# Performance work log

Measured on AMD Instinct MI355X. Metric: run time of the kernel, lower is better.

The kernel has to match this reference:

```python
import jax, jax.numpy as jnp
import numpy as np

EPS = 1e-12
TEMPERATURE = 0.1
QUEUE_SIZE = 1024
CUTOFF_KM = 25.0
EARTH_R_KM = 6371.0088


def _normalize(x, axis=-1):
    n = jnp.linalg.norm(x, axis=axis, keepdims=True)
    return x / jnp.maximum(n, EPS)


def _haversine_km(a, b):
    # a: (B,1,2), b: (1,S,2) in degrees (lat, lon) -> (B,S) km
    ra, rb = jnp.deg2rad(a), jnp.deg2rad(b)
    dlat = rb[..., 0] - ra[..., 0]
    dlon = rb[..., 1] - ra[..., 1]
    h = jnp.sin(dlat / 2) ** 2 + jnp.cos(ra[..., 0]) * jnp.cos(rb[..., 0]) * jnp.sin(dlon / 2) ** 2
    return 2.0 * EARTH_R_KM * jnp.arcsin(jnp.sqrt(jnp.clip(h, 0.0, 1.0)))


def setup_inputs() -> dict:
    key = jax.random.key(0)
    k1, k2, k3, k4, k5 = jax.random.split(key, 5)
    A, B, F, S = 3, 256, 512, 100000
    V = jax.random.normal(k1, (A, B, F), dtype=jnp.float32)
    L = jax.random.normal(k2, (B, F), dtype=jnp.float32)
    # gps as (lat, lon) degrees
    gps = jax.random.uniform(k3, (B, 2), dtype=jnp.float32) * jnp.array([120.0, 360.0]) - jnp.array([60.0, 180.0])
    support_feats = jax.random.normal(k4, (S, F), dtype=jnp.float32)
    support_gps = jax.random.uniform(k5, (S, 2), dtype=jnp.float32) * jnp.array([120.0, 360.0]) - jnp.array([60.0, 180.0])
    return {"V": V, "L": L, "gps": gps, "support_feats": support_feats, "support_gps": support_gps}


def reference(V, L, gps, support_feats, support_gps):
    T, Q = TEMPERATURE, QUEUE_SIZE
    L_norm = _normalize(L, axis=1)                      # (B,F)
    org = _normalize(V[0] * L_norm, axis=1)             # (B,F)
    aug = _normalize(V[1:] * L_norm, axis=2)            # (A-1,B,F)

    # nearest_neighbours (no_grad): per-batch NN in support set by dot-product sim
    sims = jnp.einsum('sf,bf->sb', support_feats, org)  # (S,B)
    nn_idx = jnp.argmax(sims, axis=0)                   # (B,)
    nn = _normalize(support_feats[nn_idx], axis=1)      # (B,F)
    nn = jax.lax.stop_gradient(nn)

    pos = jnp.exp(jnp.einsum('abf,bf->ab', aug, nn) / T)  # (A-1,B)
    batch_den = jnp.sum(pos, axis=0)                       # (B,)

    # nn_negative_queue (no_grad): first Q support rows farther than 25 km, zeros if fewer
    dist = _haversine_km(gps[:, None, :], support_gps[None, :, :])  # (B,S)
    far = dist > CUTOFF_KM                                          # (B,S)
    order = jnp.argsort(jnp.logical_not(far), axis=1)[:, :Q]        # stable: far rows first, in order
    valid = jnp.take_along_axis(far, order, axis=1)                 # (B,Q)
    negq = jnp.where(valid[..., None], support_feats[order], 0.0)   # (B,Q,F)
    negq = jax.lax.stop_gradient(_normalize(negq, axis=2))          # zero rows stay zero

    queue_den = jnp.sum(jnp.exp(jnp.einsum('bqf,bf->bq', negq, nn) / T), axis=1)  # (B,)

    loss = jnp.mean(-batch_den / (batch_den + queue_den))
    return loss
```

## Files before the change

kernel.cpp:

```cpp
#include <hip/hip_runtime.h>
#include <hip/hip_bf16.h>
#include <math.h>

#define B_N 256
#define F_N 512
#define S_N 100000
#define Q_N 1024
#define EPSF 1e-12f
#define BM 128
#define NBLK ((S_N + BM - 1) / BM)

typedef __attribute__((ext_vector_type(8))) short short8v;
typedef __attribute__((ext_vector_type(4))) float f32x4;

__device__ __forceinline__ unsigned short f2bf(float x) {
  unsigned u = __float_as_uint(x);
  u = u + 0x7FFFu + ((u >> 16) & 1u);
  return (unsigned short)(u >> 16);
}
__device__ __forceinline__ float bf2f(unsigned short h) {
  return __uint_as_float(((unsigned)h) << 16);
}

__device__ __forceinline__ float warpReduceSum(float v) {
  #pragma unroll
  for (int o = 32; o > 0; o >>= 1) v += __shfl_down(v, o);
  return v;
}

__device__ __forceinline__ float blockReduceSum256(float v, float* buf) {
  v = warpReduceSum(v);
  int lane = threadIdx.x & 63, w = threadIdx.x >> 6;
  __syncthreads();
  if (lane == 0) buf[w] = v;
  __syncthreads();
  return buf[0] + buf[1] + buf[2] + buf[3];
}

__device__ __forceinline__ void async_copy16(void* lds, const void* g) {
  __builtin_amdgcn_global_load_lds(
      (const __attribute__((address_space(1))) unsigned int*)g,
      (__attribute__((address_space(3))) unsigned int*)lds, 16, 0, 0);
}

__device__ __forceinline__ void cvt8(const float4 a, const float4 b,
                                     short8v& hi, short8v& lo) {
  union { unsigned u[4]; short8v v; } H, L;
  float xs[8] = {a.x, a.y, a.z, a.w, b.x, b.y, b.z, b.w};
  #pragma unroll
  for (int i = 0; i < 4; ++i) {
    float p = xs[2 * i], q = xs[2 * i + 1];
    union { __hip_bfloat162 b2; unsigned u; } c;
    c.b2 = __float22bfloat162_rn(make_float2(p, q));
    H.u[i] = c.u;
    float rp = p - __uint_as_float(c.u << 16);
    float rq = q - __uint_as_float(c.u & 0xFFFF0000u);
    union { __hip_bfloat162 b2; unsigned u; } d;
    d.b2 = __float22bfloat162_rn(make_float2(rp, rq));
    L.u[i] = d.u;
  }
  hi = H.v; lo = L.v;
}

__global__ __launch_bounds__(256) void k_prep(const float* __restrict__ V,
    const float* __restrict__ L, unsigned short* __restrict__ orgst,
    float* __restrict__ aug) {
  __shared__ float buf[4];
  int b = blockIdx.x, t = threadIdx.x;
  const float2 lv = *(const float2*)&L[b * F_N + t * 2];
  float ss = blockReduceSum256(lv.x * lv.x + lv.y * lv.y, buf);
  float invL = 1.0f / fmaxf(sqrtf(ss), EPSF);
  float lnx = lv.x * invL, lny = lv.y * invL;
  #pragma unroll
  for (int a = 0; a < 3; ++a) {
    const float2 vv = *(const float2*)&V[(a * B_N + b) * F_N + t * 2];
    float yx = vv.x * lnx, yy = vv.y * lny;
    float s2 = blockReduceSum256(yx * yx + yy * yy, buf);
    float inv = 1.0f / fmaxf(sqrtf(s2), EPSF);
    if (a == 0) {
      float ox = yx * inv, oy = yy * inv;
      int f = t * 2;
      int kt = f >> 5, kk = f & 31, sub = kk >> 3, pos = kk & 7;
      unsigned short hx = f2bf(ox), hy = f2bf(oy);
      unsigned short lx = f2bf(ox - bf2f(hx)), ly = f2bf(oy - bf2f(hy));
      int base = kt * 16384 + b * 64;
      ushort2 hv; hv.x = hx; hv.y = hy;
      ushort2 lw; lw.x = lx; lw.y = ly;
      *(ushort2*)&orgst[base + ((sub ^ (b & 7)) << 3) + pos] = hv;
      *(ushort2*)&orgst[base + (((sub | 4) ^ (b & 7)) << 3) + pos] = lw;
    } else {
      float* dst = &aug[((a - 1) * B_N + b) * F_N + t * 2];
      dst[0] = yx * inv;
      dst[1] = yy * inv;
    }
  }
}

__global__ __launch_bounds__(256, 2) void k_sims(const float* __restrict__ support,
    const unsigned short* __restrict__ orgst, unsigned long long* __restrict__ keys) {
  __shared__ __align__(16) unsigned char smem[65536];

  int t = threadIdx.x;
  int lane = t & 63, w = t >> 6;
  int r15 = lane & 15, ks = lane >> 4;
  int s0 = blockIdx.x * BM;

  f32x4 acc0[16], acc1[16];
  #pragma unroll
  for (int n = 0; n < 16; ++n) {
    acc0[n] = (f32x4){0.f, 0.f, 0.f, 0.f};
    acc1[n] = (f32x4){0.f, 0.f, 0.f, 0.f};
  }

  int row0 = s0 + w * 32 + r15;
  int row1 = row0 + 16;
  if (row0 > S_N - 1) row0 = S_N - 1;
  if (row1 > S_N - 1) row1 = S_N - 1;
  const float* ap0 = support + (size_t)row0 * F_N + ks * 8;
  const float* ap1 = support + (size_t)row1 * F_N + ks * 8;

  {
    const unsigned char* src = (const unsigned char*)orgst + t * 16;
    unsigned char* dst = smem + t * 16;
    #pragma unroll
    for (int p = 0; p < 8; ++p) async_copy16(dst + p * 4096, src + p * 4096);
  }
  float4 a0a = *(const float4*)(ap0);
  float4 a0b = *(const float4*)(ap0 + 4);
  float4 a1a = *(const float4*)(ap1);
  float4 a1b = *(const float4*)(ap1 + 4);
  __syncthreads();

  const int hioff = (ks ^ (r15 & 7)) << 4;
  const int looff = ((ks | 4) ^ (r15 & 7)) << 4;

  #pragma unroll 1
  for (int kt = 0; kt < 16; ++kt) {
    const int cur = kt & 1;
    unsigned char* bbuf = smem + cur * 32768;
    if (kt < 15) {
      const unsigned char* src =
          (const unsigned char*)orgst + (kt + 1) * 32768 + t * 16;
      unsigned char* dst = smem + (cur ^ 1) * 32768 + t * 16;
      #pragma unroll
      for (int p = 0; p < 8; ++p) async_copy16(dst + p * 4096, src + p * 4096);
    }
    short8v ah0, al0, ah1, al1;
    cvt8(a0a, a0b, ah0, al0);
    cvt8(a1a, a1b, ah1, al1);
    if (kt < 15) {
      a0a = *(const float4*)(ap0 + (kt + 1) * 32);
      a0b = *(const float4*)(ap0 + (kt + 1) * 32 + 4);
      a1a = *(const float4*)(ap1 + (kt + 1) * 32);
      a1b = *(const float4*)(ap1 + (kt + 1) * 32 + 4);
    }
    const unsigned char* bp = bbuf + r15 * 128 + hioff;
    const unsigned char* bq = bbuf + r15 * 128 + looff;
    #pragma unroll
    for (int n = 0; n < 16; ++n) {
      short8v bh = *(const short8v*)(bp + n * 2048);
      short8v bl = *(const short8v*)(bq + n * 2048);
      acc0[n] = __builtin_amdgcn_mfma_f32_16x16x32_bf16(ah0, bh, acc0[n], 0, 0, 0);
      acc1[n] = __builtin_amdgcn_mfma_f32_16x16x32_bf16(ah1, bh, acc1[n], 0, 0, 0);
      acc0[n] = __builtin_amdgcn_mfma_f32_16x16x32_bf16(al0, bh, acc0[n], 0, 0, 0);
      acc1[n] = __builtin_amdgcn_mfma_f32_16x16x32_bf16(al1, bh, acc1[n], 0, 0, 0);
      acc0[n] = __builtin_amdgcn_mfma_f32_16x16x32_bf16(ah0, bl, acc0[n], 0, 0, 0);
      acc1[n] = __builtin_amdgcn_mfma_f32_16x16x32_bf16(ah1, bl, acc1[n], 0, 0, 0);
    }
    __syncthreads();
  }

  unsigned long long* wk = (unsigned long long*)smem;
  #pragma unroll
  for (int n = 0; n < 16; ++n) {
    float bv = -INFINITY;
    int bi = 0x7FFFFFFF;
    #pragma unroll
    for (int r = 0; r < 4; ++r) {
      int sA = s0 + w * 32 + ks * 4 + r;
      float vA = acc0[n][r];
      if (sA < S_N && (vA > bv || (vA == bv && sA < bi))) { bv = vA; bi = sA; }
      int sB = sA + 16;
      float vB = acc1[n][r];
      if (sB < S_N && (vB > bv || (vB == bv && sB < bi))) { bv = vB; bi = sB; }
    }
    #pragma unroll
    for (int mask = 16; mask <= 32; mask <<= 1) {
      float ov = __shfl_xor(bv, mask);
      int oi = __shfl_xor(bi, mask);
      if (ov > bv || (ov == bv && oi < bi)) { bv = ov; bi = oi; }
    }
    if (lane < 16) {
      unsigned u = __float_as_uint(bv);
      u = (u & 0x80000000u) ? ~u : (u | 0x80000000u);
      wk[w * 256 + n * 16 + lane] =
          ((unsigned long long)u << 32) |
          (unsigned long long)(0xFFFFFFFFu - (unsigned)bi);
    }
  }
  __syncthreads();
  {
    unsigned long long k0 = wk[t], k1 = wk[256 + t];
    unsigned long long k2 = wk[512 + t], k3 = wk[768 + t];
    unsigned long long m01 = k0 > k1 ? k0 : k1;
    unsigned long long m23 = k2 > k3 ? k2 : k3;
    atomicMax(&keys[t], m01 > m23 ? m01 : m23);
  }
}

__global__ __launch_bounds__(256) void k_nn(const float* __restrict__ support,
    const unsigned long long* __restrict__ keys, const float* __restrict__ aug,
    float* __restrict__ nn, float* __restrict__ bden) {
  __shared__ float buf[4];
  int b = blockIdx.x, t = threadIdx.x;
  int idx = (int)(0xFFFFFFFFu - (unsigned)(keys[b] & 0xFFFFFFFFull));
  const float2 rv = *(const float2*)&support[(size_t)idx * F_N + t * 2];
  float ss = blockReduceSum256(rv.x * rv.x + rv.y * rv.y, buf);
  float inv = 1.0f / fmaxf(sqrtf(ss), EPSF);
  float nx = rv.x * inv, ny = rv.y * inv;
  nn[b * F_N + t * 2] = nx;
  nn[b * F_N + t * 2 + 1] = ny;
  const float2 a0 = *(const float2*)&aug[(0 * B_N + b) * F_N + t * 2];
  const float2 a1 = *(const float2*)&aug[(1 * B_N + b) * F_N + t * 2];
  float d0 = blockReduceSum256(a0.x * nx + a0.y * ny, buf);
  float d1 = blockReduceSum256(a1.x * nx + a1.y * ny, buf);
  if (t == 0) bden[b] = expf(d0 * 10.0f) + expf(d1 * 10.0f);
}

__global__ __launch_bounds__(256) void k_qdot(const float* __restrict__ support,
    const float* __restrict__ gps, const float* __restrict__ sgps,
    const float* __restrict__ nn, double* __restrict__ qpart) {
  __shared__ float nns[F_N];
  __shared__ int qi[256];
  __shared__ int wtot[4];
  __shared__ double wacc[4];
  int b = blockIdx.x >> 2, c = blockIdx.x & 3;
  int t = threadIdx.x;
  int lane = t & 63, w = t >> 6;

  *(float2*)&nns[t * 2] = *(const float2*)&nn[b * F_N + t * 2];

  const float DEG2RAD = 0.017453292519943295f;
  float la = gps[b * 2] * DEG2RAD;
  float lo = gps[b * 2 + 1] * DEG2RAD;
  float ca = cosf(la);
  double xd = 25.0 / (2.0 * 6371.0088);
  float hcut = (float)(sin(xd) * sin(xd));

  int cnt = 0;
  int qlo = c * 256;
  for (int base = 0; base < S_N; base += 256) {
    int s = base + t;
    bool far = false;
    if (s < S_N) {
      float lb = sgps[s * 2] * DEG2RAD;
      float ob = sgps[s * 2 + 1] * DEG2RAD;
      float sl = sinf((lb - la) * 0.5f);
      float so = sinf((ob - lo) * 0.5f);
      float h = sl * sl + ca * cosf(lb) * so * so;
      far = h > hcut;
    }
    unsigned long long m = __ballot(far);
    if (lane == 0) wtot[w] = (int)__popcll(m);
    __syncthreads();
    int offs = cnt;
    for (int wi = 0; wi < w; ++wi) offs += wtot[wi];
    if (far) {
      int pos = offs + (int)__popcll(m & ((1ull << lane) - 1ull));
      int rel = pos - qlo;
      if (rel >= 0 && rel < 256) qi[rel] = s;
    }
    cnt += wtot[0] + wtot[1] + wtot[2] + wtot[3];
    __syncthreads();
    if (cnt >= Q_N) break;
  }
  int nvalid = cnt < Q_N ? cnt : Q_N;
  __syncthreads();

  double acc = 0.0;
  for (int j = 0; j < 64; ++j) {
    int q = qlo + w * 64 + j;
    if (q >= nvalid) break;
    int row = qi[w * 64 + j];
    const float4* rp = (const float4*)&support[(size_t)row * F_N + lane * 8];
    float4 r0 = rp[0], r1 = rp[1];
    const float4 n0 = *(const float4*)&nns[lane * 8];
    const float4 n1 = *(const float4*)&nns[lane * 8 + 4];
    float dot = r0.x * n0.x + r0.y * n0.y + r0.z * n0.z + r0.w * n0.w +
                r1.x * n1.x + r1.y * n1.y + r1.z * n1.z + r1.w * n1.w;
    float ssq = r0.x * r0.x + r0.y * r0.y + r0.z * r0.z + r0.w * r0.w +
                r1.x * r1.x + r1.y * r1.y + r1.z * r1.z + r1.w * r1.w;
    #pragma unroll
    for (int o = 32; o > 0; o >>= 1) {
      dot += __shfl_xor(dot, o);
      ssq += __shfl_xor(ssq, o);
    }
    float val = dot / fmaxf(sqrtf(ssq), EPSF);
    acc += (double)expf(val * 10.0f);
  }
  if (lane == 0) wacc[w] = acc;
  __syncthreads();
  if (t == 0) {
    int got = nvalid - qlo;
    if (got < 0) got = 0; if (got > 256) got = 256;
    int inval = 256 - got;
    qpart[blockIdx.x] = wacc[0] + wacc[1] + wacc[2] + wacc[3] + (double)inval;
  }
}

__global__ __launch_bounds__(256) void k_final(const double* __restrict__ qpart,
    const float* __restrict__ bden, float* __restrict__ out) {
  __shared__ double buf[4];
  int t = threadIdx.x;
  double qd = qpart[t * 4] + qpart[t * 4 + 1] + qpart[t * 4 + 2] + qpart[t * 4 + 3];
  double bd = (double)bden[t];
  double v = -bd / (bd + qd);
  #pragma unroll
  for (int o = 32; o > 0; o >>= 1) v += __shfl_down(v, o);
  if ((t & 63) == 0) buf[t >> 6] = v;
  __syncthreads();
  if (t == 0) out[0] = (float)((buf[0] + buf[1] + buf[2] + buf[3]) / 256.0);
}

extern "C" void kernel_launch(void* const* d_in, const int* in_sizes, int n_in,
                              void* d_out, int out_size, void* d_ws, size_t ws_size,
                              hipStream_t stream) {
  const float* V = (const float*)d_in[0];
  const float* L = (const float*)d_in[1];
  const float* gps = (const float*)d_in[2];
  const float* support = (const float*)d_in[3];
  const float* sgps = (const float*)d_in[4];
  float* out = (float*)d_out;

  char* ws = (char*)d_ws;
  unsigned long long* keys = (unsigned long long*)ws;
  float* bden = (float*)(ws + 2048);
  double* qpart = (double*)(ws + 4096);
  unsigned short* orgst = (unsigned short*)(ws + 12288);
  float* aug = (float*)(ws + 12288 + 524288);
  float* nn = (float*)(ws + 12288 + 524288 + 1048576);

  hipMemsetAsync(keys, 0, 256 * sizeof(unsigned long long), stream);
  k_prep<<<256, 256, 0, stream>>>(V, L, orgst, aug);
  k_sims<<<NBLK, 256, 0, stream>>>(support, orgst, keys);
  k_nn<<<256, 256, 0, stream>>>(support, keys, aug, nn, bden);
  k_qdot<<<1024, 256, 0, stream>>>(support, gps, sgps, nn, qpart);
  k_final<<<1, 256, 0, stream>>>(qpart, bden, out);
}
```

Measured before the change: 167.3 us.

## Retile similarity GEMM into 512-thread blocks with mixed row-tile sizes

The support×org similarity kernel moves to 512-thread blocks whose 8 waves form a 4×2 grid over rows and batch columns. Each wave now handles 4 (or 2) 16-row slices against half the batch columns, so every B fragment read from shared memory feeds more MFMAs. The grid mixes 256-row and 128-row blocks (526 in total) so the work spreads more evenly over the CUs than the previous 782 uniform 128-row blocks. The argmax epilogue and the cross-wave reduction are reworked to match the new wave layout. Larger blocks may reduce occupancy, and the tail of smaller blocks is an extra scheduling risk.

```diff
diff --git a/kernel.cpp b/kernel.cpp
--- a/kernel.cpp
+++ b/kernel.cpp
@@ -7,8 +7,6 @@
 #define S_N 100000
 #define Q_N 1024
 #define EPSF 1e-12f
-#define BM 128
-#define NBLK ((S_N + BM - 1) / BM)
 
 typedef __attribute__((ext_vector_type(8))) short short8v;
 typedef __attribute__((ext_vector_type(4))) float f32x4;
@@ -96,39 +94,41 @@
   }
 }
 
-__global__ __launch_bounds__(256, 2) void k_sims(const float* __restrict__ support,
-    const unsigned short* __restrict__ orgst, unsigned long long* __restrict__ keys) {
-  __shared__ __align__(16) unsigned char smem[65536];
-
+template<int NM>
+__device__ __forceinline__ void sims_body(const float* __restrict__ support,
+    const unsigned short* __restrict__ orgst, unsigned long long* __restrict__ keys,
+    unsigned char* smem, int s0) {
   int t = threadIdx.x;
   int lane = t & 63, w = t >> 6;
+  int wm = w >> 1, wn = w & 1;
   int r15 = lane & 15, ks = lane >> 4;
-  int s0 = blockIdx.x * BM;
-
-  f32x4 acc0[16], acc1[16];
-  #pragma unroll
-  for (int n = 0; n < 16; ++n) {
-    acc0[n] = (f32x4){0.f, 0.f, 0.f, 0.f};
-    acc1[n] = (f32x4){0.f, 0.f, 0.f, 0.f};
-  }
-
-  int row0 = s0 + w * 32 + r15;
-  int row1 = row0 + 16;
-  if (row0 > S_N - 1) row0 = S_N - 1;
-  if (row1 > S_N - 1) row1 = S_N - 1;
-  const float* ap0 = support + (size_t)row0 * F_N + ks * 8;
-  const float* ap1 = support + (size_t)row1 * F_N + ks * 8;
+
+  f32x4 acc[NM][8];
+  #pragma unroll
+  for (int m = 0; m < NM; ++m)
+    #pragma unroll
+    for (int n = 0; n < 8; ++n) acc[m][n] = (f32x4){0.f, 0.f, 0.f, 0.f};
+
+  const float* ap[NM];
+  #pragma unroll
+  for (int m = 0; m < NM; ++m) {
+    int row = s0 + wm * (NM * 16) + m * 16 + r15;
+    if (row > S_N - 1) row = S_N - 1;
+    ap[m] = support + (size_t)row * F_N + ks * 8;
+  }
 
   {
     const unsigned char* src = (const unsigned char*)orgst + t * 16;
     unsigned char* dst = smem + t * 16;
     #pragma unroll
-    for (int p = 0; p < 8; ++p) async_copy16(dst + p * 4096, src + p * 4096);
-  }
-  float4 a0a = *(const float4*)(ap0);
-  float4 a0b = *(const float4*)(ap0 + 4);
-  float4 a1a = *(const float4*)(ap1);
-  float4 a1b = *(const float4*)(ap1 + 4);
+    for (int p = 0; p < 4; ++p) async_copy16(dst + p * 8192, src + p * 8192);
+  }
+  float4 a[NM][2];
+  #pragma unroll
+  for (int m = 0; m < NM; ++m) {
+    a[m][0] = *(const float4*)(ap[m]);
+    a[m][1] = *(const float4*)(ap[m] + 4);
+  }
   __syncthreads();
 
   const int hioff = (ks ^ (r15 & 7)) << 4;
@@ -143,47 +143,47 @@
           (const unsigned char*)orgst + (kt + 1) * 32768 + t * 16;
       unsigned char* dst = smem + (cur ^ 1) * 32768 + t * 16;
       #pragma unroll
-      for (int p = 0; p < 8; ++p) async_copy16(dst + p * 4096, src + p * 4096);
-    }
-    short8v ah0, al0, ah1, al1;
-    cvt8(a0a, a0b, ah0, al0);
-    cvt8(a1a, a1b, ah1, al1);
+      for (int p = 0; p < 4; ++p) async_copy16(dst + p * 8192, src + p * 8192);
+    }
+    short8v ah[NM], al[NM];
+    #pragma unroll
+    for (int m = 0; m < NM; ++m) cvt8(a[m][0], a[m][1], ah[m], al[m]);
     if (kt < 15) {
-      a0a = *(const float4*)(ap0 + (kt + 1) * 32);
-      a0b = *(const float4*)(ap0 + (kt + 1) * 32 + 4);
-      a1a = *(const float4*)(ap1 + (kt + 1) * 32);
-      a1b = *(const float4*)(ap1 + (kt + 1) * 32 + 4);
-    }
-    const unsigned char* bp = bbuf + r15 * 128 + hioff;
-    const unsigned char* bq = bbuf + r15 * 128 + looff;
-    #pragma unroll
-    for (int n = 0; n < 16; ++n) {
+      #pragma unroll
+      for (int m = 0; m < NM; ++m) {
+        a[m][0] = *(const float4*)(ap[m] + (kt + 1) * 32);
+        a[m][1] = *(const float4*)(ap[m] + (kt + 1) * 32 + 4);
+      }
+    }
+    const unsigned char* bp = bbuf + wn * 16384 + r15 * 128 + hioff;
+    const unsigned char* bq = bbuf + wn * 16384 + r15 * 128 + looff;
+    #pragma unroll
+    for (int n = 0; n < 8; ++n) {
       short8v bh = *(const short8v*)(bp + n * 2048);
       short8v bl = *(const short8v*)(bq + n * 2048);
-      acc0[n] = __builtin_amdgcn_mfma_f32_16x16x32_bf16(ah0, bh, acc0[n], 0, 0, 0);
-      acc1[n] = __builtin_amdgcn_mfma_f32_16x16x32_bf16(ah1, bh, acc1[n], 0, 0, 0);
-      acc0[n] = __builtin_amdgcn_mfma_f32_16x16x32_bf16(al0, bh, acc0[n], 0, 0, 0);
-      acc1[n] = __builtin_amdgcn_mfma_f32_16x16x32_bf16(al1, bh, acc1[n], 0, 0, 0);
-      acc0[n] = __builtin_amdgcn_mfma_f32_16x16x32_bf16(ah0, bl, acc0[n], 0, 0, 0);
-      acc1[n] = __builtin_amdgcn_mfma_f32_16x16x32_bf16(ah1, bl, acc1[n], 0, 0, 0);
+      #pragma unroll
+      for (int m = 0; m < NM; ++m) {
+        acc[m][n] = __builtin_amdgcn_mfma_f32_16x16x32_bf16(ah[m], bh, acc[m][n], 0, 0, 0);
+        acc[m][n] = __builtin_amdgcn_mfma_f32_16x16x32_bf16(al[m], bh, acc[m][n], 0, 0, 0);
+        acc[m][n] = __builtin_amdgcn_mfma_f32_16x16x32_bf16(ah[m], bl, acc[m][n], 0, 0, 0);
+      }
     }
     __syncthreads();
   }
 
   unsigned long long* wk = (unsigned long long*)smem;
   #pragma unroll
-  for (int n = 0; n < 16; ++n) {
+  for (int n = 0; n < 8; ++n) {
     float bv = -INFINITY;
     int bi = 0x7FFFFFFF;
     #pragma unroll
-    for (int r = 0; r < 4; ++r) {
-      int sA = s0 + w * 32 + ks * 4 + r;
-      float vA = acc0[n][r];
-      if (sA < S_N && (vA > bv || (vA == bv && sA < bi))) { bv = vA; bi = sA; }
-      int sB = sA + 16;
-      float vB = acc1[n][r];
-      if (sB < S_N && (vB > bv || (vB == bv && sB < bi))) { bv = vB; bi = sB; }
-    }
+    for (int m = 0; m < NM; ++m)
+      #pragma unroll
+      for (int r = 0; r < 4; ++r) {
+        int s = s0 + wm * (NM * 16) + m * 16 + ks * 4 + r;
+        float v = acc[m][n][r];
+        if (s < S_N && (v > bv || (v == bv && s < bi))) { bv = v; bi = s; }
+      }
     #pragma unroll
     for (int mask = 16; mask <= 32; mask <<= 1) {
       float ov = __shfl_xor(bv, mask);
@@ -193,18 +193,32 @@
     if (lane < 16) {
       unsigned u = __float_as_uint(bv);
       u = (u & 0x80000000u) ? ~u : (u | 0x80000000u);
-      wk[w * 256 + n * 16 + lane] =
+      wk[w * 128 + n * 16 + lane] =
           ((unsigned long long)u << 32) |
           (unsigned long long)(0xFFFFFFFFu - (unsigned)bi);
     }
   }
   __syncthreads();
-  {
-    unsigned long long k0 = wk[t], k1 = wk[256 + t];
-    unsigned long long k2 = wk[512 + t], k3 = wk[768 + t];
-    unsigned long long m01 = k0 > k1 ? k0 : k1;
-    unsigned long long m23 = k2 > k3 ? k2 : k3;
-    atomicMax(&keys[t], m01 > m23 ? m01 : m23);
+  if (t < 256) {
+    int p = t >> 7, c7 = t & 127;
+    unsigned long long mx = 0;
+    #pragma unroll
+    for (int i = 0; i < 4; ++i) {
+      unsigned long long k = wk[(i * 2 + p) * 128 + c7];
+      if (k > mx) mx = k;
+    }
+    atomicMax(&keys[t], mx);
+  }
+}
+
+__global__ __launch_bounds__(512, 2) void k_sims(const float* __restrict__ support,
+    const unsigned short* __restrict__ orgst, unsigned long long* __restrict__ keys) {
+  __shared__ __align__(16) unsigned char smem[65536];
+  int bid = blockIdx.x;
+  if (bid < 256) {
+    sims_body<4>(support, orgst, keys, smem, bid * 256);
+  } else {
+    sims_body<2>(support, orgst, keys, smem, 65536 + (bid - 256) * 128);
   }
 }
 
@@ -342,7 +356,7 @@
 
   hipMemsetAsync(keys, 0, 256 * sizeof(unsigned long long), stream);
   k_prep<<<256, 256, 0, stream>>>(V, L, orgst, aug);
-  k_sims<<<NBLK, 256, 0, stream>>>(support, orgst, keys);
+  k_sims<<<526, 512, 0, stream>>>(support, orgst, keys);
   k_nn<<<256, 256, 0, stream>>>(support, keys, aug, nn, bden);
   k_qdot<<<1024, 256, 0, stream>>>(support, gps, sgps, nn, qpart);
   k_final<<<1, 256, 0, stream>>>(qpart, bden, out);
```

Measured after the change: 191.0 us. 1.14x slower.

## Deepen A-operand prefetch in k_sims and fold key memset into k_prep

Applied to the files above, without the earlier changes.

Reworks the k_sims main loop so the support-row A operands are prefetched two k-steps ahead using two register sets, with a manually unrolled pair of steps. The full __syncthreads is replaced by explicit vmcnt waits and s_barrier calls, fenced by sched_barrier. The aim is to hide global-load latency behind the MFMA work. The hipMemsetAsync of the argmax keys is removed and k_prep zeroes them instead, saving one launch. In exchange it uses more registers and depends on hand-counted vmcnt values, which could be wrong if the compiler emits the loads differently.

```diff
diff --git a/kernel.cpp b/kernel.cpp
--- a/kernel.cpp
+++ b/kernel.cpp
@@ -64,9 +64,10 @@
 
 __global__ __launch_bounds__(256) void k_prep(const float* __restrict__ V,
     const float* __restrict__ L, unsigned short* __restrict__ orgst,
-    float* __restrict__ aug) {
+    float* __restrict__ aug, unsigned long long* __restrict__ keys) {
   __shared__ float buf[4];
   int b = blockIdx.x, t = threadIdx.x;
+  if (t == 0) keys[b] = 0ull;
   const float2 lv = *(const float2*)&L[b * F_N + t * 2];
   float ss = blockReduceSum256(lv.x * lv.x + lv.y * lv.y, buf);
   float invL = 1.0f / fmaxf(sqrtf(ss), EPSF);
@@ -119,56 +120,79 @@
   const float* ap0 = support + (size_t)row0 * F_N + ks * 8;
   const float* ap1 = support + (size_t)row1 * F_N + ks * 8;
 
+  const unsigned char* bsrc = (const unsigned char*)orgst + t * 16;
+
+  float4 aA0, aA1, aA2, aA3, aB0, aB1, aB2, aB3;
+
   {
-    const unsigned char* src = (const unsigned char*)orgst + t * 16;
     unsigned char* dst = smem + t * 16;
     #pragma unroll
-    for (int p = 0; p < 8; ++p) async_copy16(dst + p * 4096, src + p * 4096);
-  }
-  float4 a0a = *(const float4*)(ap0);
-  float4 a0b = *(const float4*)(ap0 + 4);
-  float4 a1a = *(const float4*)(ap1);
-  float4 a1b = *(const float4*)(ap1 + 4);
-  __syncthreads();
+    for (int p = 0; p < 8; ++p) async_copy16(dst + p * 4096, bsrc + p * 4096);
+  }
+  __builtin_amdgcn_sched_barrier(0);
+  aA0 = *(const float4*)(ap0);      aA1 = *(const float4*)(ap0 + 4);
+  aA2 = *(const float4*)(ap1);      aA3 = *(const float4*)(ap1 + 4);
+  aB0 = *(const float4*)(ap0 + 32); aB1 = *(const float4*)(ap0 + 36);
+  aB2 = *(const float4*)(ap1 + 32); aB3 = *(const float4*)(ap1 + 36);
+  __builtin_amdgcn_sched_barrier(0);
+  asm volatile("s_waitcnt vmcnt(8)" ::: "memory");
+  __builtin_amdgcn_s_barrier();
+  __builtin_amdgcn_sched_barrier(0);
 
   const int hioff = (ks ^ (r15 & 7)) << 4;
   const int looff = ((ks | 4) ^ (r15 & 7)) << 4;
 
+  #define KT_STEP(KT, R0, R1, R2, R3)                                          \
+    do {                                                                        \
+      const int kt_ = (KT);                                                     \
+      unsigned char* bbuf = smem + (kt_ & 1) * 32768;                           \
+      short8v ah0, al0, ah1, al1;                                               \
+      cvt8(R0, R1, ah0, al0);                                                   \
+      cvt8(R2, R3, ah1, al1);                                                   \
+      if (kt_ < 15) {                                                           \
+        const unsigned char* src = bsrc + (kt_ + 1) * 32768;                    \
+        unsigned char* dst = smem + ((kt_ + 1) & 1) * 32768 + t * 16;           \
+        _Pragma("unroll")                                                       \
+        for (int p = 0; p < 8; ++p) async_copy16(dst + p * 4096, src + p * 4096);\
+      }                                                                         \
+      __builtin_amdgcn_sched_barrier(0);                                        \
+      if (kt_ < 14) {                                                           \
+        R0 = *(const float4*)(ap0 + (kt_ + 2) * 32);                            \
+        R1 = *(const float4*)(ap0 + (kt_ + 2) * 32 + 4);                        \
+        R2 = *(const float4*)(ap1 + (kt_ + 2) * 32);                            \
+        R3 = *(const float4*)(ap1 + (kt_ + 2) * 32 + 4);                        \
+      }                                                                         \
+      __builtin_amdgcn_sched_barrier(0);                                        \
+      const unsigned char* bp = bbuf + r15 * 128 + hioff;                       \
+      const unsigned char* bq = bbuf + r15 * 128 + looff;                       \
+      _Pragma("unroll")                                                         \
+      for (int n = 0; n < 16; ++n) {                                            \
+        short8v bh = *(const short8v*)(bp + n * 2048);                          \
+        short8v bl = *(const short8v*)(bq + n * 2048);                          \
+        acc0[n] = __builtin_amdgcn_mfma_f32_16x16x32_bf16(ah0, bh, acc0[n], 0, 0, 0); \
+        acc1[n] = __builtin_amdgcn_mfma_f32_16x16x32_bf16(ah1, bh, acc1[n], 0, 0, 0); \
+        acc0[n] = __builtin_amdgcn_mfma_f32_16x16x32_bf16(al0, bh, acc0[n], 0, 0, 0); \
+        acc1[n] = __builtin_amdgcn_mfma_f32_16x16x32_bf16(al1, bh, acc1[n], 0, 0, 0); \
+        acc0[n] = __builtin_amdgcn_mfma_f32_16x16x32_bf16(ah0, bl, acc0[n], 0, 0, 0); \
+        acc1[n] = __builtin_amdgcn_mfma_f32_16x16x32_bf16(ah1, bl, acc1[n], 0, 0, 0); \
+      }                                                                         \
+      __builtin_amdgcn_sched_barrier(0);                                        \
+      if (kt_ < 14) {                                                           \
+        asm volatile("s_waitcnt vmcnt(4)" ::: "memory");                        \
+        __builtin_amdgcn_s_barrier();                                           \
+      } else if (kt_ == 14) {                                                   \
+        asm volatile("s_waitcnt vmcnt(0)" ::: "memory");                        \
+        __builtin_amdgcn_s_barrier();                                           \
+      }                                                                         \
+      __builtin_amdgcn_sched_barrier(0);                                        \
+    } while (0)
+
   #pragma unroll 1
-  for (int kt = 0; kt < 16; ++kt) {
-    const int cur = kt & 1;
-    unsigned char* bbuf = smem + cur * 32768;
-    if (kt < 15) {
-      const unsigned char* src =
-          (const unsigned char*)orgst + (kt + 1) * 32768 + t * 16;
-      unsigned char* dst = smem + (cur ^ 1) * 32768 + t * 16;
-      #pragma unroll
-      for (int p = 0; p < 8; ++p) async_copy16(dst + p * 4096, src + p * 4096);
-    }
-    short8v ah0, al0, ah1, al1;
-    cvt8(a0a, a0b, ah0, al0);
-    cvt8(a1a, a1b, ah1, al1);
-    if (kt < 15) {
-      a0a = *(const float4*)(ap0 + (kt + 1) * 32);
-      a0b = *(const float4*)(ap0 + (kt + 1) * 32 + 4);
-      a1a = *(const float4*)(ap1 + (kt + 1) * 32);
-      a1b = *(const float4*)(ap1 + (kt + 1) * 32 + 4);
-    }
-    const unsigned char* bp = bbuf + r15 * 128 + hioff;
-    const unsigned char* bq = bbuf + r15 * 128 + looff;
-    #pragma unroll
-    for (int n = 0; n < 16; ++n) {
-      short8v bh = *(const short8v*)(bp + n * 2048);
-      short8v bl = *(const short8v*)(bq + n * 2048);
-      acc0[n] = __builtin_amdgcn_mfma_f32_16x16x32_bf16(ah0, bh, acc0[n], 0, 0, 0);
-      acc1[n] = __builtin_amdgcn_mfma_f32_16x16x32_bf16(ah1, bh, acc1[n], 0, 0, 0);
-      acc0[n] = __builtin_amdgcn_mfma_f32_16x16x32_bf16(al0, bh, acc0[n], 0, 0, 0);
-      acc1[n] = __builtin_amdgcn_mfma_f32_16x16x32_bf16(al1, bh, acc1[n], 0, 0, 0);
-      acc0[n] = __builtin_amdgcn_mfma_f32_16x16x32_bf16(ah0, bl, acc0[n], 0, 0, 0);
-      acc1[n] = __builtin_amdgcn_mfma_f32_16x16x32_bf16(ah1, bl, acc1[n], 0, 0, 0);
-    }
-    __syncthreads();
-  }
+  for (int kt2 = 0; kt2 < 16; kt2 += 2) {
+    KT_STEP(kt2,     aA0, aA1, aA2, aA3);
+    KT_STEP(kt2 + 1, aB0, aB1, aB2, aB3);
+  }
+  #undef KT_STEP
 
   unsigned long long* wk = (unsigned long long*)smem;
   #pragma unroll
@@ -340,8 +364,7 @@
   float* aug = (float*)(ws + 12288 + 524288);
   float* nn = (float*)(ws + 12288 + 524288 + 1048576);
 
-  hipMemsetAsync(keys, 0, 256 * sizeof(unsigned long long), stream);
-  k_prep<<<256, 256, 0, stream>>>(V, L, orgst, aug);
+  k_prep<<<256, 256, 0, stream>>>(V, L, orgst, aug, keys);
   k_sims<<<NBLK, 256, 0, stream>>>(support, orgst, keys);
   k_nn<<<256, 256, 0, stream>>>(support, keys, aug, nn, bden);
   k_qdot<<<1024, 256, 0, stream>>>(support, gps, sgps, nn, qpart);
```

After: 163.8 us. 1.02x faster.
